# Kernel optimization log

Hardware: AMD Instinct MI355X
Metric: run time of the kernel (lower is better)

Reference implementation:

```python
import jax, jax.numpy as jnp
import numpy as np

COEFF = 0.97  # de-emphasis coefficient (module init kwarg)


def setup_inputs() -> dict:
    key = jax.random.key(0)
    waveform = jax.random.normal(key, (32, 2, 480000), dtype=jnp.float32)
    return {"waveform": waveform}


def reference(waveform) -> jnp.ndarray:
    # y[n] = x[n] + COEFF * y[n-1] along the last axis.
    # Expressed as a first-order linear recurrence y_n = a_n*y_{n-1} + b_n
    # with a_n = COEFF (constant), b_n = x[n], solved with a log-depth
    # associative scan: (a1,b1) o (a2,b2) = (a1*a2, a2*b1 + b2).
    a = jnp.full_like(waveform, COEFF)

    def combine(left, right):
        a_l, b_l = left
        a_r, b_r = right
        return (a_l * a_r, a_r * b_l + b_r)

    _, y = jax.lax.associative_scan(combine, (a, waveform), axis=-1)
    return y
```

## Files before the change

kernel.cpp:

```cpp
#include <hip/hip_runtime.h>


#define COEFF 0.97f
#define ROW_LEN 480000
#define HALO 512
#define SPAN_W 256
#define P_HALO (HALO / SPAN_W)
#define P_OUT 16
#define P_TOT (P_OUT + P_HALO)
#define OUT_W (P_OUT * SPAN_W)
#define WPR ((ROW_LEN + OUT_W - 1) / OUT_W)
#define BLOCK 256
#define WAVES (BLOCK / 64)
#define PF 3

typedef float v4f __attribute__((ext_vector_type(4)));

constexpr float fpow(float b, int n) {
    float r = 1.0f;
    for (int i = 0; i < n; ++i) r *= b;
    return r;
}
constexpr float W4   = fpow(COEFF, 4);
constexpr float W8   = fpow(COEFF, 8);
constexpr float W16  = fpow(COEFF, 16);
constexpr float W32  = fpow(COEFF, 32);
constexpr float W64  = fpow(COEFF, 64);
constexpr float W128 = fpow(COEFF, 128);
constexpr float W256 = fpow(COEFF, 256);
constexpr float C1P  = fpow(COEFF, 1);
constexpr float C2P  = fpow(COEFF, 2);
constexpr float C3P  = fpow(COEFF, 3);
constexpr float C4P  = fpow(COEFF, 4);

__global__ __launch_bounds__(BLOCK, 8) void deemph_kernel(const float* __restrict__ x,
                                                          float* __restrict__ y) {
    const int lane = threadIdx.x & 63;
    const int wave = threadIdx.x >> 6;
    const int widx = blockIdx.x * WAVES + wave;
    if (widx >= WPR) return;
    const int row  = blockIdx.y;

    const float* __restrict__ xrow = x + (long long)row * ROW_LEN;
    float* __restrict__ yrow       = y + (long long)row * ROW_LEN;

    const int le = widx * OUT_W - HALO + 4 * lane;

    float Aex = 1.0f;
    if (lane & 1)  Aex *= W4;
    if (lane & 2)  Aex *= W8;
    if (lane & 4)  Aex *= W16;
    if (lane & 8)  Aex *= W32;
    if (lane & 16) Aex *= W64;
    if (lane & 32) Aex *= W128;

    v4f r[PF];
    #pragma unroll
    for (int p = 0; p < PF; ++p) {
        const int e = le + p * SPAN_W;
        v4f v = {0.0f, 0.0f, 0.0f, 0.0f};
        if (e >= 0 && e < ROW_LEN) v = *(const v4f*)(xrow + e);
        r[p] = v;
    }

    float c = 0.0f;
    #pragma unroll
    for (int p = 0; p < P_TOT; ++p) {
        v4f v = r[p % PF];
        if (p + PF < P_TOT) {
            const int e2 = le + (p + PF) * SPAN_W;
            v4f nv = {0.0f, 0.0f, 0.0f, 0.0f};
            if (e2 >= 0 && e2 < ROW_LEN) nv = *(const v4f*)(xrow + e2);
            r[p % PF] = nv;
        }

        const float l0 = v.x;
        const float l1 = fmaf(COEFF, l0, v.y);
        const float l2 = fmaf(COEFF, l1, v.z);
        const float l3 = fmaf(COEFF, l2, v.w);

        float Bv = l3, Bp;
        Bp = __shfl_up(Bv, 1);  if (lane >= 1)  Bv = fmaf(W4,   Bp, Bv);
        Bp = __shfl_up(Bv, 2);  if (lane >= 2)  Bv = fmaf(W8,   Bp, Bv);
        Bp = __shfl_up(Bv, 4);  if (lane >= 4)  Bv = fmaf(W16,  Bp, Bv);
        Bp = __shfl_up(Bv, 8);  if (lane >= 8)  Bv = fmaf(W32,  Bp, Bv);
        Bp = __shfl_up(Bv, 16); if (lane >= 16) Bv = fmaf(W64,  Bp, Bv);
        Bp = __shfl_up(Bv, 32); if (lane >= 32) Bv = fmaf(W128, Bp, Bv);
        float Bex = __shfl_up(Bv, 1);
        if (lane == 0) Bex = 0.0f;
        const float B63 = __shfl(Bv, 63);

        const float Kt = fmaf(c, Aex, Bex);
        c = fmaf(c, W256, B63);

        if (p >= P_HALO) {
            const int e = le + p * SPAN_W;
            if (e < ROW_LEN) {
                v4f o;
                o.x = fmaf(Kt, C1P, l0);
                o.y = fmaf(Kt, C2P, l1);
                o.z = fmaf(Kt, C3P, l2);
                o.w = fmaf(Kt, C4P, l3);
                *(v4f*)(yrow + e) = o;
            }
        }
    }
}

extern "C" void kernel_launch(void* const* d_in, const int* in_sizes, int n_in,
                              void* d_out, int out_size, void* d_ws, size_t ws_size,
                              hipStream_t stream) {
    (void)n_in; (void)d_ws; (void)ws_size; (void)out_size;
    const float* x = (const float*)d_in[0];
    float* y = (float*)d_out;
    const int n_rows = in_sizes[0] / ROW_LEN;
    dim3 grid((WPR + WAVES - 1) / WAVES, n_rows);
    deemph_kernel<<<grid, BLOCK, 0, stream>>>(x, y);
}
```

Measured before the change: 217.4 us.

## Give each lane a 16-element segment and shrink the halo to one span

```diff
diff --git a/kernel.cpp b/kernel.cpp
--- a/kernel.cpp
+++ b/kernel.cpp
@@ -3,16 +3,15 @@
 
 #define COEFF 0.97f
 #define ROW_LEN 480000
-#define HALO 512
-#define SPAN_W 256
-#define P_HALO (HALO / SPAN_W)
-#define P_OUT 16
+#define SEG 16
+#define CPT (SEG / 4)
+#define SPAN_W (64 * SEG)
+#define P_HALO 1
+#define P_OUT 8
 #define P_TOT (P_OUT + P_HALO)
 #define OUT_W (P_OUT * SPAN_W)
 #define WPR ((ROW_LEN + OUT_W - 1) / OUT_W)
-#define BLOCK 256
-#define WAVES (BLOCK / 64)
-#define PF 3
+#define PF 2
 
 typedef float v4f __attribute__((ext_vector_type(4)));
 
@@ -21,87 +20,102 @@
     for (int i = 0; i < n; ++i) r *= b;
     return r;
 }
-constexpr float W4   = fpow(COEFF, 4);
-constexpr float W8   = fpow(COEFF, 8);
-constexpr float W16  = fpow(COEFF, 16);
-constexpr float W32  = fpow(COEFF, 32);
-constexpr float W64  = fpow(COEFF, 64);
-constexpr float W128 = fpow(COEFF, 128);
-constexpr float W256 = fpow(COEFF, 256);
-constexpr float C1P  = fpow(COEFF, 1);
-constexpr float C2P  = fpow(COEFF, 2);
-constexpr float C3P  = fpow(COEFF, 3);
-constexpr float C4P  = fpow(COEFF, 4);
+constexpr float S0 = fpow(COEFF, SEG * 1);
+constexpr float S1 = fpow(COEFF, SEG * 2);
+constexpr float S2 = fpow(COEFF, SEG * 4);
+constexpr float S3 = fpow(COEFF, SEG * 8);
+constexpr float S4 = fpow(COEFF, SEG * 16);
+constexpr float S5 = fpow(COEFF, SEG * 32);
+constexpr float CP = fpow(COEFF, SPAN_W);
 
-__global__ __launch_bounds__(BLOCK, 8) void deemph_kernel(const float* __restrict__ x,
-                                                          float* __restrict__ y) {
-    const int lane = threadIdx.x & 63;
-    const int wave = threadIdx.x >> 6;
-    const int widx = blockIdx.x * WAVES + wave;
-    if (widx >= WPR) return;
+struct Pows { float p[SEG + 1]; };
+constexpr Pows make_pows() {
+    Pows P{};
+    float r = 1.0f;
+    for (int i = 0; i <= SEG; ++i) { P.p[i] = r; r *= COEFF; }
+    return P;
+}
+constexpr Pows PW = make_pows();
+
+__global__ __launch_bounds__(64, 4) void deemph_kernel(const float* __restrict__ x,
+                                                       float* __restrict__ y) {
+    const int lane = threadIdx.x;
+    const int widx = blockIdx.x;
     const int row  = blockIdx.y;
 
     const float* __restrict__ xrow = x + (long long)row * ROW_LEN;
     float* __restrict__ yrow       = y + (long long)row * ROW_LEN;
 
-    const int le = widx * OUT_W - HALO + 4 * lane;
+    const int lbase = widx * OUT_W - P_HALO * SPAN_W + SEG * lane;
 
     float Aex = 1.0f;
-    if (lane & 1)  Aex *= W4;
-    if (lane & 2)  Aex *= W8;
-    if (lane & 4)  Aex *= W16;
-    if (lane & 8)  Aex *= W32;
-    if (lane & 16) Aex *= W64;
-    if (lane & 32) Aex *= W128;
+    if (lane & 1)  Aex *= S0;
+    if (lane & 2)  Aex *= S1;
+    if (lane & 4)  Aex *= S2;
+    if (lane & 8)  Aex *= S3;
+    if (lane & 16) Aex *= S4;
+    if (lane & 32) Aex *= S5;
 
-    v4f r[PF];
+    v4f rb[PF][CPT];
     #pragma unroll
-    for (int p = 0; p < PF; ++p) {
-        const int e = le + p * SPAN_W;
-        v4f v = {0.0f, 0.0f, 0.0f, 0.0f};
-        if (e >= 0 && e < ROW_LEN) v = *(const v4f*)(xrow + e);
-        r[p] = v;
+    for (int q = 0; q < PF; ++q) {
+        #pragma unroll
+        for (int cc = 0; cc < CPT; ++cc) {
+            const int e = lbase + q * SPAN_W + 4 * cc;
+            v4f v = {0.0f, 0.0f, 0.0f, 0.0f};
+            if (e >= 0 && e < ROW_LEN) v = *(const v4f*)(xrow + e);
+            rb[q][cc] = v;
+        }
     }
 
     float c = 0.0f;
     #pragma unroll
     for (int p = 0; p < P_TOT; ++p) {
-        v4f v = r[p % PF];
+        float l[SEG];
+        #pragma unroll
+        for (int cc = 0; cc < CPT; ++cc) {
+            v4f v = rb[p % PF][cc];
+            l[4*cc+0] = v.x; l[4*cc+1] = v.y; l[4*cc+2] = v.z; l[4*cc+3] = v.w;
+        }
         if (p + PF < P_TOT) {
-            const int e2 = le + (p + PF) * SPAN_W;
-            v4f nv = {0.0f, 0.0f, 0.0f, 0.0f};
-            if (e2 >= 0 && e2 < ROW_LEN) nv = *(const v4f*)(xrow + e2);
-            r[p % PF] = nv;
+            #pragma unroll
+            for (int cc = 0; cc < CPT; ++cc) {
+                const int e = lbase + (p + PF) * SPAN_W + 4 * cc;
+                v4f v = {0.0f, 0.0f, 0.0f, 0.0f};
+                if (e >= 0 && e < ROW_LEN) v = *(const v4f*)(xrow + e);
+                rb[p % PF][cc] = v;
+            }
         }
 
-        const float l0 = v.x;
-        const float l1 = fmaf(COEFF, l0, v.y);
-        const float l2 = fmaf(COEFF, l1, v.z);
-        const float l3 = fmaf(COEFF, l2, v.w);
+        #pragma unroll
+        for (int i = 1; i < SEG; ++i) l[i] = fmaf(COEFF, l[i-1], l[i]);
 
-        float Bv = l3, Bp;
-        Bp = __shfl_up(Bv, 1);  if (lane >= 1)  Bv = fmaf(W4,   Bp, Bv);
-        Bp = __shfl_up(Bv, 2);  if (lane >= 2)  Bv = fmaf(W8,   Bp, Bv);
-        Bp = __shfl_up(Bv, 4);  if (lane >= 4)  Bv = fmaf(W16,  Bp, Bv);
-        Bp = __shfl_up(Bv, 8);  if (lane >= 8)  Bv = fmaf(W32,  Bp, Bv);
-        Bp = __shfl_up(Bv, 16); if (lane >= 16) Bv = fmaf(W64,  Bp, Bv);
-        Bp = __shfl_up(Bv, 32); if (lane >= 32) Bv = fmaf(W128, Bp, Bv);
+        float Bv = l[SEG-1], Bp;
+        Bp = __shfl_up(Bv, 1);  if (lane >= 1)  Bv = fmaf(S0, Bp, Bv);
+        Bp = __shfl_up(Bv, 2);  if (lane >= 2)  Bv = fmaf(S1, Bp, Bv);
+        Bp = __shfl_up(Bv, 4);  if (lane >= 4)  Bv = fmaf(S2, Bp, Bv);
+        Bp = __shfl_up(Bv, 8);  if (lane >= 8)  Bv = fmaf(S3, Bp, Bv);
+        Bp = __shfl_up(Bv, 16); if (lane >= 16) Bv = fmaf(S4, Bp, Bv);
+        Bp = __shfl_up(Bv, 32); if (lane >= 32) Bv = fmaf(S5, Bp, Bv);
         float Bex = __shfl_up(Bv, 1);
         if (lane == 0) Bex = 0.0f;
         const float B63 = __shfl(Bv, 63);
 
         const float Kt = fmaf(c, Aex, Bex);
-        c = fmaf(c, W256, B63);
+        c = fmaf(c, CP, B63);
 
         if (p >= P_HALO) {
-            const int e = le + p * SPAN_W;
-            if (e < ROW_LEN) {
-                v4f o;
-                o.x = fmaf(Kt, C1P, l0);
-                o.y = fmaf(Kt, C2P, l1);
-                o.z = fmaf(Kt, C3P, l2);
-                o.w = fmaf(Kt, C4P, l3);
-                *(v4f*)(yrow + e) = o;
+            #pragma unroll
+            for (int cc = 0; cc < CPT; ++cc) {
+                const int e = lbase + p * SPAN_W + 4 * cc;
+                if (e < ROW_LEN) {
+                    v4f o;
+                    o.x = fmaf(Kt, PW.p[4*cc+1], l[4*cc+0]);
+                    o.y = fmaf(Kt, PW.p[4*cc+2], l[4*cc+1]);
+                    o.z = fmaf(Kt, PW.p[4*cc+3], l[4*cc+2]);
+                    o.w = fmaf(Kt, PW.p[4*cc+4], l[4*cc+3]);
+                    *(v4f*)(yrow + e) = o;
+                }
             }
         }
     }
@@ -114,6 +128,6 @@
     const float* x = (const float*)d_in[0];
     float* y = (float*)d_out;
     const int n_rows = in_sizes[0] / ROW_LEN;
-    dim3 grid((WPR + WAVES - 1) / WAVES, n_rows);
-    deemph_kernel<<<grid, BLOCK, 0, stream>>>(x, y);
+    dim3 grid(WPR, n_rows);
+    deemph_kernel<<<grid, 64, 0, stream>>>(x, y);
 }
```

Result: slower. 231.7 us (+6.6%).
